# Kernel optimization log

Hardware: AMD Instinct MI355X
Metric: run time of the kernel (lower is better)

Reference implementation:

```python
import jax, jax.numpy as jnp
import numpy as np


def setup_inputs() -> dict:
    key = jax.random.key(0)
    k1, k2 = jax.random.split(key)
    x = jax.random.normal(k1, (32, 128, 64, 64), dtype=jnp.float32)
    weight = jax.random.normal(k2, (256, 128, 3, 3), dtype=jnp.float32)
    return {"x": x, "weight": weight}


def reference(x, weight):
    # Batched VALID cross-correlation, stride 1 (same math as the triple loop
    # of single-channel conv2d calls summed over in_channels).
    # x: [B, Cin, H, W]; weight: [Cout, Cin, k, k] -> out: [B, Cout, H-k+1, W-k+1]
    return jax.lax.conv_general_dilated(
        x, weight,
        window_strides=(1, 1),
        padding="VALID",
        dimension_numbers=("NCHW", "OIHW", "NCHW"),
    )
```

## Files before the change

### kernel.cpp

```cpp
#include <hip/hip_runtime.h>


using bf16x8 = __attribute__((ext_vector_type(8))) __bf16;
using f32x4  = __attribute__((ext_vector_type(4))) float;

constexpr int CIN  = 128;
constexpr int HW   = 64;
constexpr int COUT = 256;
constexpr int OW   = 62;
constexpr int NS   = 62 * 62;
constexpr int NTOT = 32 * NS;
constexpr int KTOT = 9 * CIN;
constexpr int BM = 256, BN = 256, BK = 64;
constexpr int NT = KTOT / BK;
constexpr int NBLK = (NTOT + BN - 1) / BN;

constexpr size_t AP_BYTES = (size_t)COUT * KTOT * 2;
constexpr size_t XP_BYTES = (size_t)32 * HW * HW * CIN * 2;
constexpr size_t WS_NEEDED = AP_BYTES + XP_BYTES;

constexpr int BUF  = 65536;
constexpr int BOFF = 32768;

__device__ __forceinline__ unsigned short f2bf(float f) {
  unsigned u = __float_as_uint(f);
  u += 0x7fffu + ((u >> 16) & 1u);
  return (unsigned short)(u >> 16);
}
__device__ __forceinline__ unsigned pack2(float a, float b) {
  return (unsigned)f2bf(a) | ((unsigned)f2bf(b) << 16);
}

__device__ __forceinline__ void gld16(const void* g, void* l) {
  __builtin_amdgcn_global_load_lds(
      (const __attribute__((address_space(1))) unsigned int*)g,
      (__attribute__((address_space(3))) unsigned int*)l, 16, 0, 0);
}


__global__ __launch_bounds__(256)
void prepack_w(const float* __restrict__ w, unsigned* __restrict__ ap32) {
  const int idx = blockIdx.x * 256 + threadIdx.x;
  const int co  = idx / 576;
  const int k2  = idx - co * 576;
  const int k   = k2 * 2;
  const int tap = k >> 7;
  const int ci  = k & 127;
  const float v0 = w[(co * 128 + ci) * 9 + tap];
  const float v1 = w[(co * 128 + ci + 1) * 9 + tap];
  ap32[idx] = pack2(v0, v1);
}

__global__ __launch_bounds__(256)
void prepack_x(const float* __restrict__ x, unsigned* __restrict__ xp32) {
  const int bh = blockIdx.x;
  const int b  = bh >> 6, h = bh & 63;
  const int t  = threadIdx.x;
  const int c  = t & 63;
  const int w0 = (t >> 6) * 16;

  const float* p0 = x + (((size_t)(b * 128 + 2 * c) * HW) + h) * HW + w0;
  const float* p1 = p0 + (size_t)HW * HW;
  float r0[16], r1[16];
#pragma unroll
  for (int j = 0; j < 4; ++j) {
    *reinterpret_cast<float4*>(&r0[j * 4]) = reinterpret_cast<const float4*>(p0)[j];
    *reinterpret_cast<float4*>(&r1[j * 4]) = reinterpret_cast<const float4*>(p1)[j];
  }
  unsigned* o = xp32 + ((size_t)bh * HW + w0) * 64 + c;
#pragma unroll
  for (int j = 0; j < 16; ++j)
    o[j * 64] = pack2(r0[j], r1[j]);
}


__global__ __launch_bounds__(512, 2)
void conv_main(const unsigned short* __restrict__ Ap,
               const unsigned short* __restrict__ Xp,
               float* __restrict__ out) {
  __shared__ __align__(16) char lds[2 * BUF];

  const int tid  = threadIdx.x;
  const int lane = tid & 63;
  const int wid  = tid >> 6;
  const int wm   = wid & 1;
  const int wn   = wid >> 1;
  const int n_base = blockIdx.x * BN;

  const int l3  = lane >> 3;
  const int sw8 = ((lane & 7) ^ l3) * 8;
  int aoff[4];
  unsigned xoff[4];
#pragma unroll
  for (int j = 0; j < 4; ++j) {
    const int r = j * 64 + wid * 8 + l3;
    aoff[j] = r * KTOT + sw8;
    unsigned n = n_base + r;
    if (n >= NTOT) n = NTOT - 1;
    const unsigned bi = n / NS;
    const unsigned s0 = n - bi * NS;
    const unsigned oh = s0 / OW;
    const unsigned ww = s0 - oh * OW;
    xoff[j] = ((bi * HW + oh) * HW + ww) * CIN + sw8;
  }

  const int fr = lane & 15;
  const int gl = lane >> 4;
  const int s0b = ((gl)     ^ (fr & 7)) * 16;
  const int s1b = ((4 + gl) ^ (fr & 7)) * 16;
  const int abase = (wm * 128 + fr) * 128;
  const int bbase = BOFF + (wn * 64 + fr) * 128;

  f32x4 acc[8][4] = {};
  bf16x8 aq[8];
  bf16x8 b0q[4], b1q[4];

  auto STAGE_A = [&](int tt, char* dst) {
#pragma unroll
    for (int j = 0; j < 4; ++j)
      gld16(Ap + aoff[j] + tt * 64, dst + (j * 64 + wid * 8) * 128);
  };
  auto STAGE_B = [&](int tt, char* dst) {
    const int tap = tt >> 1;
    const int kh  = tap / 3;
    const int kw  = tap - kh * 3;
    const int xk  = (kh * HW + kw) * CIN + (tt & 1) * 64;
#pragma unroll
    for (int j = 0; j < 4; ++j)
      gld16(Xp + xoff[j] + xk, dst + BOFF + (j * 64 + wid * 8) * 128);
  };

  auto LOAD_A = [&](const char* cur, int mq) {
#pragma unroll
    for (int mi = 0; mi < 4; ++mi) {
      aq[mi * 2 + 0] = *reinterpret_cast<const bf16x8*>(cur + abase + mq * 8192 + mi * 2048 + s0b);
      aq[mi * 2 + 1] = *reinterpret_cast<const bf16x8*>(cur + abase + mq * 8192 + mi * 2048 + s1b);
    }
  };
  auto LOAD_B = [&](const char* cur, int nq, bf16x8* bq) {
#pragma unroll
    for (int ni = 0; ni < 2; ++ni) {
      bq[ni * 2 + 0] = *reinterpret_cast<const bf16x8*>(cur + bbase + nq * 4096 + ni * 2048 + s0b);
      bq[ni * 2 + 1] = *reinterpret_cast<const bf16x8*>(cur + bbase + nq * 4096 + ni * 2048 + s1b);
    }
  };
  auto MFMA16 = [&](int mq, int nq, const bf16x8* bq) {
    __builtin_amdgcn_s_setprio(1);
#pragma unroll
    for (int mi = 0; mi < 4; ++mi)
#pragma unroll
      for (int ni = 0; ni < 2; ++ni)
#pragma unroll
        for (int kk = 0; kk < 2; ++kk)
          acc[mq * 4 + mi][nq * 2 + ni] = __builtin_amdgcn_mfma_f32_16x16x32_bf16(
              aq[mi * 2 + kk], bq[ni * 2 + kk], acc[mq * 4 + mi][nq * 2 + ni], 0, 0, 0);
    __builtin_amdgcn_s_setprio(0);
  };

  STAGE_A(0, lds);
  STAGE_B(0, lds);

#pragma unroll
  for (int t = 0; t < NT; ++t) {
    char* cur = lds + (t & 1) * BUF;
    char* nxt = lds + ((t + 1) & 1) * BUF;

    if (t < NT - 1) {
      STAGE_A(t + 1, nxt);
      asm volatile("s_waitcnt vmcnt(4)" ::: "memory");
    } else {
      asm volatile("s_waitcnt vmcnt(0)" ::: "memory");
    }
    __builtin_amdgcn_s_barrier();
    __builtin_amdgcn_sched_barrier(0);
    LOAD_A(cur, 0);
    LOAD_B(cur, 0, b0q);
    asm volatile("s_waitcnt lgkmcnt(0)" ::: "memory");
    __builtin_amdgcn_sched_barrier(0);
    MFMA16(0, 0, b0q);
    __builtin_amdgcn_s_barrier();

    LOAD_B(cur, 1, b1q);
    if (t < NT - 1) STAGE_B(t + 1, nxt);
    __builtin_amdgcn_s_barrier();
    asm volatile("s_waitcnt lgkmcnt(0)" ::: "memory");
    __builtin_amdgcn_sched_barrier(0);
    MFMA16(0, 1, b1q);
    __builtin_amdgcn_s_barrier();

    LOAD_A(cur, 1);
    __builtin_amdgcn_s_barrier();
    asm volatile("s_waitcnt lgkmcnt(0)" ::: "memory");
    __builtin_amdgcn_sched_barrier(0);
    MFMA16(1, 1, b1q);
    __builtin_amdgcn_s_barrier();

    MFMA16(1, 0, b0q);
    __builtin_amdgcn_s_barrier();
  }

#pragma unroll
  for (int ni = 0; ni < 4; ++ni) {
    const unsigned n = n_base + wn * 64 + ni * 16 + fr;
    if (n >= NTOT) continue;
    const unsigned b2 = n / NS;
    const unsigned s2 = n - b2 * NS;
    float* op = out + (size_t)b2 * (COUT * NS) + s2
                    + (size_t)(wm * 128 + gl * 4) * NS;
#pragma unroll
    for (int mi = 0; mi < 8; ++mi)
#pragma unroll
      for (int r = 0; r < 4; ++r)
        op[(mi * 16 + r) * NS] = acc[mi][ni][r];
  }
}


__global__ __launch_bounds__(256)
void conv_fallback(const float* __restrict__ x, const float* __restrict__ w,
                   float* __restrict__ out) {
  __shared__ __align__(16) unsigned short As[128 * 32];
  __shared__ __align__(16) unsigned short Bs[128 * 32];

  const int t    = threadIdx.x;
  const int lane = t & 63;
  const int wid  = t >> 6;
  const int wm   = wid >> 1;
  const int wn   = wid & 1;
  const int co_base = blockIdx.x * 128;
  const int n_base  = blockIdx.y * 128;

  const int bn  = t & 127;
  const int bg0 = t >> 7;
  const unsigned n0   = n_base + bn;
  const unsigned bidx = n0 / NS;
  const unsigned s0   = n0 - bidx * NS;
  const unsigned oh   = s0 / OW;
  const unsigned ow   = s0 - oh * OW;
  const float* xb = x + (bidx * (CIN * HW * HW) + oh * HW + ow);

  const int am  = t & 127;
  const int ag0 = (t >> 7) * 2;
  const float* wb = w + (co_base + am) * KTOT;

  f32x4 acc[4][4] = {};

  for (int ks = 0; ks < 36; ++ks) {
    const int tap = ks >> 2;
    const int ci0 = (ks & 3) * 32;
    const int kh  = tap / 3;
    const int kw  = tap - kh * 3;
    const int xo  = kh * HW + kw;

    float av[2][8], bv[2][8];
#pragma unroll
    for (int gi = 0; gi < 2; ++gi) {
      const int g = ag0 + gi;
#pragma unroll
      for (int j = 0; j < 8; ++j)
        av[gi][j] = wb[(ci0 + g * 8 + j) * 9 + tap];
    }
#pragma unroll
    for (int gi = 0; gi < 2; ++gi) {
      const int g = bg0 + gi * 2;
#pragma unroll
      for (int j = 0; j < 8; ++j)
        bv[gi][j] = xb[xo + (ci0 + g * 8 + j) * (HW * HW)];
    }

    __syncthreads();

#pragma unroll
    for (int gi = 0; gi < 2; ++gi) {
      const int g = ag0 + gi;
      uint4 pv;
      pv.x = pack2(av[gi][0], av[gi][1]);
      pv.y = pack2(av[gi][2], av[gi][3]);
      pv.z = pack2(av[gi][4], av[gi][5]);
      pv.w = pack2(av[gi][6], av[gi][7]);
      *reinterpret_cast<uint4*>(&As[am * 32 + ((g ^ ((am >> 1) & 3)) << 3)]) = pv;
    }
#pragma unroll
    for (int gi = 0; gi < 2; ++gi) {
      const int g = bg0 + gi * 2;
      uint4 pv;
      pv.x = pack2(bv[gi][0], bv[gi][1]);
      pv.y = pack2(bv[gi][2], bv[gi][3]);
      pv.z = pack2(bv[gi][4], bv[gi][5]);
      pv.w = pack2(bv[gi][6], bv[gi][7]);
      *reinterpret_cast<uint4*>(&Bs[bn * 32 + ((g ^ ((bn >> 1) & 3)) << 3)]) = pv;
    }

    __syncthreads();

    bf16x8 af[4], bfr[4];
    const int g = lane >> 4;
#pragma unroll
    for (int mi = 0; mi < 4; ++mi) {
      const int m = wm * 64 + mi * 16 + (lane & 15);
      af[mi] = *reinterpret_cast<const bf16x8*>(&As[m * 32 + ((g ^ ((m >> 1) & 3)) << 3)]);
    }
#pragma unroll
    for (int ni = 0; ni < 4; ++ni) {
      const int nn = wn * 64 + ni * 16 + (lane & 15);
      bfr[ni] = *reinterpret_cast<const bf16x8*>(&Bs[nn * 32 + ((g ^ ((nn >> 1) & 3)) << 3)]);
    }
#pragma unroll
    for (int mi = 0; mi < 4; ++mi)
#pragma unroll
      for (int ni = 0; ni < 4; ++ni)
        acc[mi][ni] = __builtin_amdgcn_mfma_f32_16x16x32_bf16(af[mi], bfr[ni],
                                                              acc[mi][ni], 0, 0, 0);
  }

#pragma unroll
  for (int ni = 0; ni < 4; ++ni) {
    const unsigned n  = n_base + wn * 64 + ni * 16 + (lane & 15);
    const unsigned b2 = n / NS;
    const unsigned s2 = n - b2 * NS;
    float* op = out + (size_t)b2 * (COUT * NS) + s2
                    + (size_t)(co_base + wm * 64 + (lane >> 4) * 4) * NS;
#pragma unroll
    for (int mi = 0; mi < 4; ++mi)
#pragma unroll
      for (int r = 0; r < 4; ++r)
        op[(mi * 16 + r) * NS] = acc[mi][ni][r];
  }
}

extern "C" void kernel_launch(void* const* d_in, const int* in_sizes, int n_in,
                              void* d_out, int out_size, void* d_ws, size_t ws_size,
                              hipStream_t stream) {
  const float* x = (const float*)d_in[0];
  const float* w = (const float*)d_in[1];
  float* out = (float*)d_out;

  if (ws_size >= WS_NEEDED) {
    unsigned* ap32 = (unsigned*)d_ws;
    unsigned short* Ap = (unsigned short*)d_ws;
    unsigned short* Xp = (unsigned short*)((char*)d_ws + AP_BYTES);
    unsigned* xp32 = (unsigned*)Xp;
    prepack_w<<<576, 256, 0, stream>>>(w, ap32);
    prepack_x<<<32 * HW, 256, 0, stream>>>(x, xp32);
    conv_main<<<dim3(NBLK), 512, 0, stream>>>(Ap, Xp, out);
  } else {
    conv_fallback<<<dim3(2, NTOT / 128), 256, 0, stream>>>(x, w, out);
  }
}
```

Measured before the change: 121.4 us.

## Split global-to-LDS staging into halves and prefetch B two tiles ahead

Global-to-LDS staging of the A and B tiles is now issued in halves spread across the four MFMA phases of each k-step. The B tile is now prefetched two iterations ahead into the current buffer once its contents have been read. The vmcnt wait moves to the end of the iteration so the next iteration's loop top needs no global-load wait. The goal is to hide global load latency behind more compute and spread memory traffic evenly. In exchange, the buffer reuse and the waitcnt counts become fragile and could race if the barriers are misplaced.

```diff
diff --git a/kernel.cpp b/kernel.cpp
--- a/kernel.cpp
+++ b/kernel.cpp
@@ -115,19 +115,23 @@
   bf16x8 aq[8];
   bf16x8 b0q[4], b1q[4];
 
-  auto STAGE_A = [&](int tt, char* dst) {
-#pragma unroll
-    for (int j = 0; j < 4; ++j)
+  auto STAGE_A_HALF = [&](int tt, int h, char* dst) {
+#pragma unroll
+    for (int jj = 0; jj < 2; ++jj) {
+      const int j = h * 2 + jj;
       gld16(Ap + aoff[j] + tt * 64, dst + (j * 64 + wid * 8) * 128);
-  };
-  auto STAGE_B = [&](int tt, char* dst) {
+    }
+  };
+  auto STAGE_B_HALF = [&](int tt, int h, char* dst) {
     const int tap = tt >> 1;
     const int kh  = tap / 3;
     const int kw  = tap - kh * 3;
     const int xk  = (kh * HW + kw) * CIN + (tt & 1) * 64;
 #pragma unroll
-    for (int j = 0; j < 4; ++j)
+    for (int jj = 0; jj < 2; ++jj) {
+      const int j = h * 2 + jj;
       gld16(Xp + xoff[j] + xk, dst + BOFF + (j * 64 + wid * 8) * 128);
+    }
   };
 
   auto LOAD_A = [&](const char* cur, int mq) {
@@ -157,31 +161,34 @@
     __builtin_amdgcn_s_setprio(0);
   };
 
-  STAGE_A(0, lds);
-  STAGE_B(0, lds);
+  {
+    char* b0 = lds;
+    char* b1 = lds + BUF;
+    STAGE_A_HALF(0, 0, b0); STAGE_A_HALF(0, 1, b0);
+    STAGE_B_HALF(0, 0, b0); STAGE_B_HALF(0, 1, b0);
+    STAGE_B_HALF(1, 0, b1); STAGE_B_HALF(1, 1, b1);
+    asm volatile("s_waitcnt vmcnt(4)" ::: "memory");
+    __builtin_amdgcn_s_barrier();
+  }
 
 #pragma unroll
   for (int t = 0; t < NT; ++t) {
-    char* cur = lds + (t & 1) * BUF;
-    char* nxt = lds + ((t + 1) & 1) * BUF;
-
-    if (t < NT - 1) {
-      STAGE_A(t + 1, nxt);
-      asm volatile("s_waitcnt vmcnt(4)" ::: "memory");
-    } else {
-      asm volatile("s_waitcnt vmcnt(0)" ::: "memory");
-    }
-    __builtin_amdgcn_s_barrier();
-    __builtin_amdgcn_sched_barrier(0);
+    const char* cur = lds + (t & 1) * BUF;
+    char* curw = lds + (t & 1) * BUF;
+    char* nxt  = lds + ((t + 1) & 1) * BUF;
+
     LOAD_A(cur, 0);
     LOAD_B(cur, 0, b0q);
+    if (t + 1 < NT) STAGE_A_HALF(t + 1, 0, nxt);
+    asm volatile("s_waitcnt lgkmcnt(8)" ::: "memory");
+    __builtin_amdgcn_s_barrier();
     asm volatile("s_waitcnt lgkmcnt(0)" ::: "memory");
     __builtin_amdgcn_sched_barrier(0);
     MFMA16(0, 0, b0q);
     __builtin_amdgcn_s_barrier();
 
     LOAD_B(cur, 1, b1q);
-    if (t < NT - 1) STAGE_B(t + 1, nxt);
+    if (t + 1 < NT) STAGE_A_HALF(t + 1, 1, nxt);
     __builtin_amdgcn_s_barrier();
     asm volatile("s_waitcnt lgkmcnt(0)" ::: "memory");
     __builtin_amdgcn_sched_barrier(0);
@@ -189,12 +196,19 @@
     __builtin_amdgcn_s_barrier();
 
     LOAD_A(cur, 1);
+    if (t + 2 < NT) STAGE_B_HALF(t + 2, 0, curw);
     __builtin_amdgcn_s_barrier();
     asm volatile("s_waitcnt lgkmcnt(0)" ::: "memory");
     __builtin_amdgcn_sched_barrier(0);
     MFMA16(1, 1, b1q);
     __builtin_amdgcn_s_barrier();
 
+    if (t + 2 < NT) STAGE_B_HALF(t + 2, 1, curw);
+    if (t + 1 < NT) {
+      if (t + 2 < NT) asm volatile("s_waitcnt vmcnt(4)" ::: "memory");
+      else            asm volatile("s_waitcnt vmcnt(0)" ::: "memory");
+    }
+    __builtin_amdgcn_s_barrier();
     MFMA16(1, 0, b0q);
     __builtin_amdgcn_s_barrier();
   }
```

Result: faster. 117.6 us (-3.1%).
